# Kernel tuning notes

Hardware: AMD Instinct MI355X
Metric: run time of the kernel (lower is better)

The kernel has to match this reference:

```python
import jax, jax.numpy as jnp
import numpy as np

N = 100000      # nodes
E = 1600000     # edges
HID = 128
NODE_IN = 32
EDGE_IN = 16
EMB = 32
VOCAB = 100000
LAYERS = 3
EPS = 1e-5


def setup_inputs() -> dict:
    key = jax.random.key(0)
    ks = jax.random.split(key, 24)
    s = 0.05
    inp = {
        "x": jax.random.normal(ks[0], (N, NODE_IN), jnp.float32),
        "edge_attr": jax.random.normal(ks[1], (E, EDGE_IN), jnp.float32),
        "naics_emb": jax.random.normal(ks[2], (VOCAB, EMB), jnp.float32) * s,
        "ln_g": jnp.ones((EMB,), jnp.float32),
        "ln_b": jnp.zeros((EMB,), jnp.float32),
        "W_in": jax.random.normal(ks[3], (EMB + NODE_IN, HID), jnp.float32) * s,
        "b_in": jnp.zeros((HID,), jnp.float32),
        "Wl": jax.random.normal(ks[4], (LAYERS, HID, HID), jnp.float32) * s,
        "bl": jnp.zeros((LAYERS, HID), jnp.float32),
        "Wr": jax.random.normal(ks[5], (LAYERS, HID, HID), jnp.float32) * s,
        "bn_g": jnp.ones((LAYERS, HID), jnp.float32),
        "bn_b": jnp.zeros((LAYERS, HID), jnp.float32),
        "We1": jax.random.normal(ks[6], (2 * HID + EDGE_IN, HID), jnp.float32) * s,
        "be1": jnp.zeros((HID,), jnp.float32),
        "We2": jax.random.normal(ks[7], (HID, HID // 2), jnp.float32) * s,
        "be2": jnp.zeros((HID // 2,), jnp.float32),
        "We3": jax.random.normal(ks[8], (HID // 2, 1), jnp.float32) * s,
        "be3": jnp.zeros((1,), jnp.float32),
        "edge_index": jax.random.randint(ks[9], (2, E), 0, N, jnp.int64 if jax.config.jax_enable_x64 else jnp.int32),
        "naics_indices": jax.random.randint(ks[10], (N,), 0, VOCAB, jnp.int64 if jax.config.jax_enable_x64 else jnp.int32),
    }
    return inp


def reference(x, edge_attr, naics_emb, ln_g, ln_b, W_in, b_in, Wl, bl, Wr,
              bn_g, bn_b, We1, be1, We2, be2, We3, be3, edge_index, naics_indices):
    # NAICS embedding + LayerNorm
    emb = naics_emb[naics_indices]                    # [N, EMB]
    mu = emb.mean(-1, keepdims=True)
    var = emb.var(-1, keepdims=True)
    emb = (emb - mu) * jax.lax.rsqrt(var + EPS) * ln_g + ln_b

    # input projection (dropout in eval mode = identity)
    h = jax.nn.relu(jnp.concatenate([emb, x], axis=1) @ W_in + b_in)  # [N, HID]
    initial = h

    row, col = edge_index[0], edge_index[1]           # src, dst (PyG: aggregate at dst)
    deg = jax.ops.segment_sum(jnp.ones((E,), h.dtype), col, num_segments=N)
    inv_deg = (1.0 / jnp.maximum(deg, 1.0))[:, None]  # [N,1]

    for i in range(LAYERS):
        # SAGEConv: lin_l(mean_j x_j) + lin_r(x_i)
        agg = jax.ops.segment_sum(h[row], col, num_segments=N) * inv_deg
        out = agg @ Wl[i] + bl[i] + h @ Wr[i]
        # BatchNorm1d (training-mode batch statistics over nodes)
        m = out.mean(0)
        v = out.var(0)
        out = (out - m) * jax.lax.rsqrt(v + EPS) * bn_g[i] + bn_b[i]
        h = jnp.tanh(out) + h                         # activation + residual
        if i % 2 == 1:
            h = h + initial

    # edge-gather MLP
    ef = jnp.concatenate([h[row], h[col], edge_attr], axis=1)  # [E, 2H+EDGE_IN]
    z = jax.nn.relu(ef @ We1 + be1)
    z = jax.nn.relu(z @ We2 + be2)
    return z @ We3 + be3                              # [E, 1]
```

## Files before the change

### kernel.cpp

```cpp
#include <hip/hip_runtime.h>
#include <hip/hip_bf16.h>
#include <cstddef>

#define HID 128
#define EMBD 32
#define NIN 32
#define EIN 16
#define EPSV 1e-5f

__device__ __forceinline__ float rlf(float v, int l) {
    return __int_as_float(__builtin_amdgcn_readlane(__float_as_int(v), l));
}

extern "C" __global__ void __launch_bounds__(256)
k_input(const float* __restrict__ x, const float* __restrict__ etab,
        const int* __restrict__ nidx, const float* __restrict__ lng_,
        const float* __restrict__ lnb_, const float* __restrict__ Win,
        const float* __restrict__ bin_, float* __restrict__ h,
        float* __restrict__ init_, int* __restrict__ zi, int* __restrict__ zc, int nn)
{
    __shared__ float Ws[64 * HID];
    __shared__ float lng[EMBD], lnb[EMBD], bin[HID];
    __shared__ float xbuf[4][64];
    if (zi) {
        int gid = blockIdx.x * blockDim.x + threadIdx.x, st = gridDim.x * blockDim.x;
        for (int i = gid; i < nn; i += st) { zi[i] = 0; zc[i] = 0; }
    }
    for (int i = threadIdx.x; i < 64 * HID; i += 256) Ws[i] = Win[i];
    if (threadIdx.x < EMBD) { lng[threadIdx.x] = lng_[threadIdx.x]; lnb[threadIdx.x] = lnb_[threadIdx.x]; }
    if (threadIdx.x < HID) bin[threadIdx.x] = bin_[threadIdx.x];
    __syncthreads();
    const int wv = threadIdx.x >> 6, lane = threadIdx.x & 63;
    const int w0 = blockIdx.x * 4 + wv, nw = gridDim.x * 4;
    for (int n = w0; n < nn; n += nw) {
        float e = 0.f;
        if (lane < EMBD) e = etab[(size_t)nidx[n] * EMBD + lane];
        float s = e, q = e * e;
        #pragma unroll
        for (int o = 16; o; o >>= 1) { s += __shfl_xor(s, o, 32); q += __shfl_xor(q, o, 32); }
        if (lane < EMBD) {
            float m = s * (1.f / EMBD);
            float v = q * (1.f / EMBD) - m * m;
            xbuf[wv][lane] = (e - m) * rsqrtf(v + EPSV) * lng[lane] + lnb[lane];
        } else {
            xbuf[wv][lane] = x[(size_t)n * NIN + (lane - NIN)];
        }
        float2 a0 = *(const float2*)&bin[2 * lane], a1 = {0.f, 0.f};
        #pragma unroll 8
        for (int k = 0; k < 64; k += 2) {
            float2 wA = *(const float2*)&Ws[k * HID + 2 * lane];
            float2 wB = *(const float2*)&Ws[(k + 1) * HID + 2 * lane];
            a0.x = fmaf(xbuf[wv][k], wA.x, a0.x);     a0.y = fmaf(xbuf[wv][k], wA.y, a0.y);
            a1.x = fmaf(xbuf[wv][k + 1], wB.x, a1.x); a1.y = fmaf(xbuf[wv][k + 1], wB.y, a1.y);
        }
        float2 r; r.x = fmaxf(a0.x + a1.x, 0.f); r.y = fmaxf(a0.y + a1.y, 0.f);
        *(float2*)&h[(size_t)n * HID + 2 * lane] = r;
        *(float2*)&init_[(size_t)n * HID + 2 * lane] = r;
    }
}

extern "C" __global__ void k_deg(const int* __restrict__ col, int* __restrict__ degi, int ne) {
    int i = blockIdx.x * blockDim.x + threadIdx.x, st = gridDim.x * blockDim.x;
    for (; i < ne; i += st) atomicAdd(&degi[col[i]], 1);
}

extern "C" __global__ void __launch_bounds__(1024)
k_scan(const int* __restrict__ degi, int* __restrict__ offs, int nn) {
    __shared__ int ps[1024];
    const int t = threadIdx.x;
    const int per = (nn + 1023) / 1024;
    const int s = min(t * per, nn), e = min(s + per, nn);
    int sum = 0;
    for (int i = s; i < e; i++) sum += degi[i];
    ps[t] = sum;
    __syncthreads();
    for (int off = 1; off < 1024; off <<= 1) {
        int v = (t >= off) ? ps[t - off] : 0;
        __syncthreads();
        ps[t] += v;
        __syncthreads();
    }
    int run = (t ? ps[t - 1] : 0);
    for (int i = s; i < e; i++) { offs[i] = run; run += degi[i]; }
    if (t == 1023) offs[nn] = run;
}

extern "C" __global__ void k_fill(const int* __restrict__ row, const int* __restrict__ col,
                                  const int* __restrict__ offs, int* __restrict__ cur,
                                  int* __restrict__ csr, int ne) {
    int i = blockIdx.x * blockDim.x + threadIdx.x, st = gridDim.x * blockDim.x;
    for (; i < ne; i += st) {
        int c = col[i];
        int p = atomicAdd(&cur[c], 1);
        csr[offs[c] + p] = row[i];
    }
}

extern "C" __global__ void __launch_bounds__(256)
k_agg(const float* __restrict__ h, const int* __restrict__ offs,
      const int* __restrict__ csr, float* __restrict__ agg,
      float* __restrict__ stats, int nn)
{
    if (blockIdx.x == 0 && threadIdx.x < 2 * HID) stats[threadIdx.x] = 0.f;
    const int lane = threadIdx.x & 63;
    int w = blockIdx.x * 4 + (threadIdx.x >> 6), nw = gridDim.x * 4;
    for (int n = w; n < nn; n += nw) {
        const int o0 = offs[n], o1 = offs[n + 1];
        float2 acc0 = {0.f, 0.f}, acc1 = {0.f, 0.f};
        int j = o0;
        for (; j + 8 <= o1; j += 8) {
            int s[8];
            #pragma unroll
            for (int i = 0; i < 8; i++) s[i] = csr[j + i];
            float2 v[8];
            #pragma unroll
            for (int i = 0; i < 8; i++) v[i] = *(const float2*)&h[(size_t)s[i] * HID + 2 * lane];
            #pragma unroll
            for (int i = 0; i < 8; i += 2) {
                acc0.x += v[i].x;     acc0.y += v[i].y;
                acc1.x += v[i + 1].x; acc1.y += v[i + 1].y;
            }
        }
        for (; j < o1; j++) {
            int s0 = csr[j];
            float2 v0 = *(const float2*)&h[(size_t)s0 * HID + 2 * lane];
            acc0.x += v0.x; acc0.y += v0.y;
        }
        const float idg = 1.f / fmaxf((float)(o1 - o0), 1.f);
        float2 r; r.x = (acc0.x + acc1.x) * idg; r.y = (acc0.y + acc1.y) * idg;
        *(float2*)&agg[(size_t)n * HID + 2 * lane] = r;
    }
}

extern "C" __global__ void k_degf(const int* __restrict__ col, float* __restrict__ deg, int ne) {
    int i = blockIdx.x * blockDim.x + threadIdx.x, st = gridDim.x * blockDim.x;
    for (; i < ne; i += st) unsafeAtomicAdd(&deg[col[i]], 1.f);
}
extern "C" __global__ void k_invdeg(const float* __restrict__ deg, float* __restrict__ inv, int nn) {
    int i = blockIdx.x * blockDim.x + threadIdx.x;
    if (i < nn) inv[i] = 1.f / fmaxf(deg[i], 1.f);
}
extern "C" __global__ void __launch_bounds__(256)
k_scatter(const float* __restrict__ h, const int* __restrict__ row,
          const int* __restrict__ col, float* agg, float* __restrict__ stats, int ne)
{
    if (blockIdx.x == 0 && threadIdx.x < 2 * HID) stats[threadIdx.x] = 0.f;
    const int lane = threadIdx.x & 63;
    int w = blockIdx.x * 4 + (threadIdx.x >> 6), nw = gridDim.x * 4;
    for (int e = w; e < ne; e += nw) {
        int r = row[e], c = col[e];
        float2 v = *(const float2*)&h[(size_t)r * HID + 2 * lane];
        unsafeAtomicAdd(&agg[(size_t)c * HID + 2 * lane], v.x);
        unsafeAtomicAdd(&agg[(size_t)c * HID + 2 * lane + 1], v.y);
    }
}

extern "C" __global__ void __launch_bounds__(512)
k_gemm(const float* __restrict__ X1, const float* __restrict__ scale,
       const float* __restrict__ W1, const float* __restrict__ X2,
       const float* __restrict__ W2, const float* __restrict__ bias,
       float* __restrict__ out, float* __restrict__ stats, int nn)
{
    __shared__ float W1s[HID * HID];
    __shared__ float W2s[HID * HID];
    const int tid = threadIdx.x;
    const bool dual = (X2 != nullptr);
    for (int i = tid; i < HID * HID / 4; i += 512) {
        ((float4*)W1s)[i] = ((const float4*)W1)[i];
        if (dual) ((float4*)W2s)[i] = ((const float4*)W2)[i];
    }
    __syncthreads();
    const int lane = tid & 63, wv = tid >> 6;
    const int gw = blockIdx.x * 8 + wv, nwv = gridDim.x * 8;
    float2 bv = {0.f, 0.f};
    if (bias) bv = *(const float2*)&bias[2 * lane];
    float2 sm = {0.f, 0.f}, sq = {0.f, 0.f};
    for (int nb = gw * 8; nb < nn; nb += nwv * 8) {
        const int nN = min(8, nn - nb);
        float2 xA[8], xB[8];
        #pragma unroll
        for (int i = 0; i < 8; i++) {
            xA[i] = {0.f, 0.f}; xB[i] = {0.f, 0.f};
            if (i < nN) {
                xA[i] = *(const float2*)&X1[(size_t)(nb + i) * HID + 2 * lane];
                if (scale) { float sc = scale[nb + i]; xA[i].x *= sc; xA[i].y *= sc; }
                if (dual) xB[i] = *(const float2*)&X2[(size_t)(nb + i) * HID + 2 * lane];
            }
        }
        float2 acc[8];
        #pragma unroll
        for (int i = 0; i < 8; i++) acc[i] = bv;
        if (dual) {
            for (int k = 0; k < HID; k += 2) {
                float2 w1a = *(const float2*)&W1s[k * HID + 2 * lane];
                float2 w1b = *(const float2*)&W1s[(k + 1) * HID + 2 * lane];
                float2 w2a = *(const float2*)&W2s[k * HID + 2 * lane];
                float2 w2b = *(const float2*)&W2s[(k + 1) * HID + 2 * lane];
                const int kl = k >> 1;
                #pragma unroll
                for (int i = 0; i < 8; i++) {
                    float sa = rlf(xA[i].x, kl), sb = rlf(xA[i].y, kl);
                    float ta = rlf(xB[i].x, kl), tb = rlf(xB[i].y, kl);
                    acc[i].x = fmaf(sa, w1a.x, acc[i].x); acc[i].y = fmaf(sa, w1a.y, acc[i].y);
                    acc[i].x = fmaf(sb, w1b.x, acc[i].x); acc[i].y = fmaf(sb, w1b.y, acc[i].y);
                    acc[i].x = fmaf(ta, w2a.x, acc[i].x); acc[i].y = fmaf(ta, w2a.y, acc[i].y);
                    acc[i].x = fmaf(tb, w2b.x, acc[i].x); acc[i].y = fmaf(tb, w2b.y, acc[i].y);
                }
            }
        } else {
            for (int k = 0; k < HID; k += 2) {
                float2 w1a = *(const float2*)&W1s[k * HID + 2 * lane];
                float2 w1b = *(const float2*)&W1s[(k + 1) * HID + 2 * lane];
                const int kl = k >> 1;
                #pragma unroll
                for (int i = 0; i < 8; i++) {
                    float sa = rlf(xA[i].x, kl), sb = rlf(xA[i].y, kl);
                    acc[i].x = fmaf(sa, w1a.x, acc[i].x); acc[i].y = fmaf(sa, w1a.y, acc[i].y);
                    acc[i].x = fmaf(sb, w1b.x, acc[i].x); acc[i].y = fmaf(sb, w1b.y, acc[i].y);
                }
            }
        }
        #pragma unroll
        for (int i = 0; i < 8; i++) {
            if (i < nN) {
                *(float2*)&out[(size_t)(nb + i) * HID + 2 * lane] = acc[i];
                sm.x += acc[i].x; sm.y += acc[i].y;
                sq.x += acc[i].x * acc[i].x; sq.y += acc[i].y * acc[i].y;
            }
        }
    }
    unsafeAtomicAdd(&stats[2 * lane],           sm.x);
    unsafeAtomicAdd(&stats[2 * lane + 1],       sm.y);
    unsafeAtomicAdd(&stats[HID + 2 * lane],     sq.x);
    unsafeAtomicAdd(&stats[HID + 2 * lane + 1], sq.y);
}

extern "C" __global__ void __launch_bounds__(256)
k_update(const float* __restrict__ outb, const float* __restrict__ stats,
         const float* __restrict__ g, const float* __restrict__ b,
         float* h, const float* __restrict__ init_, int addinit, int n4, float invn)
{
    __shared__ float scsh[2 * HID];
    if (threadIdx.x < HID) {
        int f = threadIdx.x;
        float m = stats[f] * invn;
        float v = stats[HID + f] * invn - m * m;
        float s = rsqrtf(v + EPSV) * g[f];
        scsh[f] = s;
        scsh[HID + f] = fmaf(-m, s, b[f]);
    }
    __syncthreads();
    int i = blockIdx.x * blockDim.x + threadIdx.x, st = gridDim.x * blockDim.x;
    for (; i < n4; i += st) {
        float4 o = ((const float4*)outb)[i];
        int f = (i & 31) * 4;
        float4 s  = *(const float4*)&scsh[f];
        float4 sh = *(const float4*)&scsh[HID + f];
        float4 hv = ((const float4*)h)[i];
        float4 r;
        r.x = tanhf(fmaf(o.x, s.x, sh.x)) + hv.x;
        r.y = tanhf(fmaf(o.y, s.y, sh.y)) + hv.y;
        r.z = tanhf(fmaf(o.z, s.z, sh.z)) + hv.z;
        r.w = tanhf(fmaf(o.w, s.w, sh.w)) + hv.w;
        if (addinit) {
            float4 iv = ((const float4*)init_)[i];
            r.x += iv.x; r.y += iv.y; r.z += iv.z; r.w += iv.w;
        }
        ((float4*)h)[i] = r;
    }
}

extern "C" __global__ void __launch_bounds__(512)
k_proj(const float* __restrict__ outb, const float* __restrict__ stats,
       const float* __restrict__ g, const float* __restrict__ b,
       const float* __restrict__ hold, const float* __restrict__ W1,
       const float* __restrict__ W2, const float* __restrict__ b1,
       float* __restrict__ outA, float* __restrict__ outB, int nn, float invn)
{
    __shared__ float W1s[HID * HID];
    __shared__ float W2s[HID * HID];
    __shared__ float scsh[2 * HID];
    const int tid = threadIdx.x;
    for (int i = tid; i < HID * HID / 4; i += 512) {
        ((float4*)W1s)[i] = ((const float4*)W1)[i];
        ((float4*)W2s)[i] = ((const float4*)W2)[i];
    }
    if (tid < HID) {
        float m = stats[tid] * invn;
        float v = stats[HID + tid] * invn - m * m;
        float s = rsqrtf(v + EPSV) * g[tid];
        scsh[tid] = s;
        scsh[HID + tid] = fmaf(-m, s, b[tid]);
    }
    __syncthreads();
    const int lane = tid & 63, wv = tid >> 6;
    const int gw = blockIdx.x * 8 + wv, nwv = gridDim.x * 8;
    const float2 sA  = *(const float2*)&scsh[2 * lane];
    const float2 shA = *(const float2*)&scsh[HID + 2 * lane];
    float2 bv = *(const float2*)&b1[2 * lane];
    for (int nb = gw * 8; nb < nn; nb += nwv * 8) {
        const int nN = min(8, nn - nb);
        float2 xH[8];
        #pragma unroll
        for (int i = 0; i < 8; i++) {
            xH[i] = {0.f, 0.f};
            if (i < nN) {
                float2 o  = *(const float2*)&outb[(size_t)(nb + i) * HID + 2 * lane];
                float2 hv = *(const float2*)&hold[(size_t)(nb + i) * HID + 2 * lane];
                xH[i].x = tanhf(fmaf(o.x, sA.x, shA.x)) + hv.x;
                xH[i].y = tanhf(fmaf(o.y, sA.y, shA.y)) + hv.y;
            }
        }
        float2 accA[8], accB[8];
        #pragma unroll
        for (int i = 0; i < 8; i++) { accA[i] = bv; accB[i] = {0.f, 0.f}; }
        for (int k = 0; k < HID; k += 2) {
            float2 w1a = *(const float2*)&W1s[k * HID + 2 * lane];
            float2 w1b = *(const float2*)&W1s[(k + 1) * HID + 2 * lane];
            float2 w2a = *(const float2*)&W2s[k * HID + 2 * lane];
            float2 w2b = *(const float2*)&W2s[(k + 1) * HID + 2 * lane];
            const int kl = k >> 1;
            #pragma unroll
            for (int i = 0; i < 8; i++) {
                float sa = rlf(xH[i].x, kl), sb = rlf(xH[i].y, kl);
                accA[i].x = fmaf(sa, w1a.x, accA[i].x); accA[i].y = fmaf(sa, w1a.y, accA[i].y);
                accA[i].x = fmaf(sb, w1b.x, accA[i].x); accA[i].y = fmaf(sb, w1b.y, accA[i].y);
                accB[i].x = fmaf(sa, w2a.x, accB[i].x); accB[i].y = fmaf(sa, w2a.y, accB[i].y);
                accB[i].x = fmaf(sb, w2b.x, accB[i].x); accB[i].y = fmaf(sb, w2b.y, accB[i].y);
            }
        }
        #pragma unroll
        for (int i = 0; i < 8; i++) {
            if (i < nN) {
                *(float2*)&outA[(size_t)(nb + i) * HID + 2 * lane] = accA[i];
                *(float2*)&outB[(size_t)(nb + i) * HID + 2 * lane] = accB[i];
            }
        }
    }
}

extern "C" __global__ void __launch_bounds__(256)
k_edge(const float* __restrict__ A, const float* __restrict__ B,
       const float* __restrict__ eattr, const int* __restrict__ row,
       const int* __restrict__ col, const float* __restrict__ We1e,
       const float* __restrict__ We2, const float* __restrict__ be2,
       const float* __restrict__ We3, const float* __restrict__ be3,
       float* __restrict__ outp, int beg, int end, int ne)
{
    __shared__ float zbuf[32][132];
    __shared__ float tbuf[4][32][8];
    const int tid = threadIdx.x, lane = tid & 63, wv = tid >> 6;
    float2 w1r[16];
    #pragma unroll
    for (int j = 0; j < 16; j++) w1r[j] = *(const float2*)&We1e[j * HID + 2 * lane];
    const int fi = lane & 7, ks = lane >> 3;
    const int f0 = 16 * wv + 2 * fi;
    float w2r0[16], w2r1[16];
    #pragma unroll
    for (int m = 0; m < 16; m++) {
        w2r0[m] = We2[(16 * ks + m) * 64 + f0];
        w2r1[m] = We2[(16 * ks + m) * 64 + f0 + 1];
    }
    const float b20 = be2[f0], b21 = be2[f0 + 1];
    const float w30 = We3[f0], w31 = We3[f0 + 1];
    const float bias3 = be3[0];
    const int wcol4 = (((lane >> 1) & 3) << 3) | ((lane >> 1) >> 2);
    const int woff = wcol4 * 4 + (lane & 1) * 2;
    for (int cb = beg + blockIdx.x * 32; cb < end; cb += gridDim.x * 32) {
        const int e0 = cb + wv * 8;
        float2 ear = {0.f, 0.f};
        if (e0 + (lane >> 3) < ne) ear = *(const float2*)&eattr[(size_t)e0 * EIN + 2 * lane];
        int rr[8], cc[8];
        #pragma unroll
        for (int i = 0; i < 8; i++) {
            const int e = e0 + i;
            rr[i] = (e < ne) ? row[e] : 0;
            cc[i] = (e < ne) ? col[e] : 0;
        }
        float2 av[8], bv8[8];
        #pragma unroll
        for (int i = 0; i < 8; i++) {
            av[i]  = *(const float2*)&A[(size_t)rr[i] * HID + 2 * lane];
            bv8[i] = *(const float2*)&B[(size_t)cc[i] * HID + 2 * lane];
        }
        float* zw = &zbuf[wv * 8][woff];
        #pragma unroll
        for (int i = 0; i < 8; i++) {
            float2 q; q.x = av[i].x + bv8[i].x; q.y = av[i].y + bv8[i].y;
            #pragma unroll
            for (int j = 0; j < 16; j++) {
                float s = rlf((j & 1) ? ear.y : ear.x, i * 8 + (j >> 1));
                q.x = fmaf(s, w1r[j].x, q.x);
                q.y = fmaf(s, w1r[j].y, q.y);
            }
            q.x = fmaxf(q.x, 0.f); q.y = fmaxf(q.y, 0.f);
            *(float2*)zw = q;
            zw += 132;
        }
        __syncthreads();
        const float* zp = &zbuf[0][ks * 4];
        #pragma unroll 2
        for (int e = 0; e < 32; e++) {
            float4 z0 = *(const float4*)(zp);
            float4 z1 = *(const float4*)(zp + 32);
            float4 z2 = *(const float4*)(zp + 64);
            float4 z3 = *(const float4*)(zp + 96);
            zp += 132;
            float acc0 = 0.f, acc1 = 0.f;
            acc0 = fmaf(z0.x, w2r0[0],  acc0); acc1 = fmaf(z0.x, w2r1[0],  acc1);
            acc0 = fmaf(z0.y, w2r0[1],  acc0); acc1 = fmaf(z0.y, w2r1[1],  acc1);
            acc0 = fmaf(z0.z, w2r0[2],  acc0); acc1 = fmaf(z0.z, w2r1[2],  acc1);
            acc0 = fmaf(z0.w, w2r0[3],  acc0); acc1 = fmaf(z0.w, w2r1[3],  acc1);
            acc0 = fmaf(z1.x, w2r0[4],  acc0); acc1 = fmaf(z1.x, w2r1[4],  acc1);
            acc0 = fmaf(z1.y, w2r0[5],  acc0); acc1 = fmaf(z1.y, w2r1[5],  acc1);
            acc0 = fmaf(z1.z, w2r0[6],  acc0); acc1 = fmaf(z1.z, w2r1[6],  acc1);
            acc0 = fmaf(z1.w, w2r0[7],  acc0); acc1 = fmaf(z1.w, w2r1[7],  acc1);
            acc0 = fmaf(z2.x, w2r0[8],  acc0); acc1 = fmaf(z2.x, w2r1[8],  acc1);
            acc0 = fmaf(z2.y, w2r0[9],  acc0); acc1 = fmaf(z2.y, w2r1[9],  acc1);
            acc0 = fmaf(z2.z, w2r0[10], acc0); acc1 = fmaf(z2.z, w2r1[10], acc1);
            acc0 = fmaf(z2.w, w2r0[11], acc0); acc1 = fmaf(z2.w, w2r1[11], acc1);
            acc0 = fmaf(z3.x, w2r0[12], acc0); acc1 = fmaf(z3.x, w2r1[12], acc1);
            acc0 = fmaf(z3.y, w2r0[13], acc0); acc1 = fmaf(z3.y, w2r1[13], acc1);
            acc0 = fmaf(z3.z, w2r0[14], acc0); acc1 = fmaf(z3.z, w2r1[14], acc1);
            acc0 = fmaf(z3.w, w2r0[15], acc0); acc1 = fmaf(z3.w, w2r1[15], acc1);
            acc0 += __shfl_xor(acc0, 8);  acc1 += __shfl_xor(acc1, 8);
            acc0 += __shfl_xor(acc0, 16); acc1 += __shfl_xor(acc1, 16);
            acc0 += __shfl_xor(acc0, 32); acc1 += __shfl_xor(acc1, 32);
            float o0 = fmaxf(acc0 + b20, 0.f), o1 = fmaxf(acc1 + b21, 0.f);
            float t3 = fmaf(o0, w30, o1 * w31);
            if (ks == 0) tbuf[wv][e][fi] = t3;
        }
        __syncthreads();
        {
            const int e = tid >> 3, p = tid & 7;
            float s = (tbuf[0][e][p] + tbuf[1][e][p]) + (tbuf[2][e][p] + tbuf[3][e][p]);
            s += __shfl_xor(s, 1); s += __shfl_xor(s, 2); s += __shfl_xor(s, 4);
            if (p == 0 && cb + e < end) outp[cb + e] = s + bias3;
        }
        __syncthreads();
    }
}

extern "C" void kernel_launch(void* const* d_in, const int* in_sizes, int n_in,
                              void* d_out, int out_size, void* d_ws, size_t ws_size,
                              hipStream_t stream)
{
    const float* x     = (const float*)d_in[0];
    const float* eattr = (const float*)d_in[1];
    const float* etab  = (const float*)d_in[2];
    const float* lng   = (const float*)d_in[3];
    const float* lnb   = (const float*)d_in[4];
    const float* Win   = (const float*)d_in[5];
    const float* bin   = (const float*)d_in[6];
    const float* Wl    = (const float*)d_in[7];
    const float* bl    = (const float*)d_in[8];
    const float* Wr    = (const float*)d_in[9];
    const float* bng   = (const float*)d_in[10];
    const float* bnb   = (const float*)d_in[11];
    const float* We1   = (const float*)d_in[12];
    const float* be1   = (const float*)d_in[13];
    const float* We2   = (const float*)d_in[14];
    const float* be2   = (const float*)d_in[15];
    const float* We3   = (const float*)d_in[16];
    const float* be3   = (const float*)d_in[17];
    const int*   eidx  = (const int*)d_in[18];
    const int*   nidx  = (const int*)d_in[19];

    const int nn = in_sizes[0] / NIN;
    const int ne = in_sizes[1] / EIN;
    const int* row = eidx;
    const int* col = eidx + ne;
    const float invn = 1.0f / nn;

    float* ws = (float*)d_ws;
    const size_t big = (size_t)nn * HID;
    float* h    = ws;
    float* bufB = ws + big;
    float* bufA = ws + 2 * big;
    float* tail = ws + 3 * big;

    const size_t need_csr = (3 * big + 3 * (size_t)nn + 1 + (size_t)ne + 512) * 4;
    const bool use_csr = (ws_size >= need_csr);

    if (use_csr) {
        int*   degi  = (int*)tail;
        int*   offs  = degi + nn;
        int*   cur   = offs + nn + 1;
        int*   csr   = cur + nn;
        float* stats = (float*)(csr + ne);

        k_input<<<512, 256, 0, stream>>>(x, etab, nidx, lng, lnb, Win, bin, h, bufB,
                                         degi, cur, nn);
        k_deg<<<1024, 256, 0, stream>>>(col, degi, ne);
        k_scan<<<1, 1024, 0, stream>>>(degi, offs, nn);
        k_fill<<<1024, 256, 0, stream>>>(row, col, offs, cur, csr, ne);

        for (int i = 0; i < 3; i++) {
            k_agg<<<2048, 256, 0, stream>>>(h, offs, csr, bufA, stats, nn);
            k_gemm<<<256, 512, 0, stream>>>(bufA, nullptr, Wl + (size_t)i * HID * HID,
                                            h, Wr + (size_t)i * HID * HID, bl + i * HID,
                                            bufA, stats, nn);
            if (i < 2) {
                k_update<<<1024, 256, 0, stream>>>(bufA, stats, bng + i * HID, bnb + i * HID,
                                                   h, bufB, i & 1, nn * HID / 4, invn);
            } else {
                k_proj<<<256, 512, 0, stream>>>(bufA, stats, bng + i * HID, bnb + i * HID,
                                                h, We1, We1 + HID * HID, be1,
                                                bufA, bufB, nn, invn);
            }
        }
    } else {
        float* deg   = tail;
        float* inv   = deg + nn;
        float* stats = inv + nn;

        k_input<<<512, 256, 0, stream>>>(x, etab, nidx, lng, lnb, Win, bin, h, bufB,
                                         nullptr, nullptr, nn);
        hipMemsetAsync(deg, 0, (size_t)nn * 4, stream);
        k_degf<<<1024, 256, 0, stream>>>(col, deg, ne);
        k_invdeg<<<(nn + 255) / 256, 256, 0, stream>>>(deg, inv, nn);

        for (int i = 0; i < 3; i++) {
            hipMemsetAsync(bufA, 0, big * 4, stream);
            k_scatter<<<2048, 256, 0, stream>>>(h, row, col, bufA, stats, ne);
            k_gemm<<<256, 512, 0, stream>>>(bufA, inv, Wl + (size_t)i * HID * HID,
                                            h, Wr + (size_t)i * HID * HID, bl + i * HID,
                                            bufA, stats, nn);
            if (i < 2) {
                k_update<<<1024, 256, 0, stream>>>(bufA, stats, bng + i * HID, bnb + i * HID,
                                                   h, bufB, i & 1, nn * HID / 4, invn);
            } else {
                k_proj<<<256, 512, 0, stream>>>(bufA, stats, bng + i * HID, bnb + i * HID,
                                                h, We1, We1 + HID * HID, be1,
                                                bufA, bufB, nn, invn);
            }
        }
    }

    const int half = (ne / 2) & ~31;
    k_edge<<<1792, 256, 0, stream>>>(bufA, bufB, eattr, row, col,
                                     We1 + 2 * HID * HID, We2, be2, We3, be3,
                                     (float*)d_out, 0, half, ne);
    k_edge<<<1792, 256, 0, stream>>>(bufA, bufB, eattr, row, col,
                                     We1 + 2 * HID * HID, We2, be2, We3, be3,
                                     (float*)d_out, half, ne, ne);
}
```

Measured before the change: 2.897 ms.

## Widen node GEMM blocks to 768 threads and re-split edge MLP second layer

The node GEMM and projection kernels go from 512 to 768 threads per block, so each block that stages the two 128x128 weight matrices in shared memory runs twelve waves instead of eight. This amortises the weight load over more rows and adds waves per CU. In the edge kernel, the second-layer work is re-split: each wave now covers 32 output features over 16 edges, each lane reduces over 32 inputs instead of 16, and one shuffle stage is dropped. The cost is more registers per lane (64 held weights) and tighter register limits at 768 threads, which could cause spills or lower occupancy.

Result: faster. 2.685 ms (-7.3%).

```diff
diff --git a/kernel.cpp b/kernel.cpp
--- a/kernel.cpp
+++ b/kernel.cpp
@@ -155,7 +155,7 @@
     }
 }
 
-extern "C" __global__ void __launch_bounds__(512)
+extern "C" __global__ void __launch_bounds__(768)
 k_gemm(const float* __restrict__ X1, const float* __restrict__ scale,
        const float* __restrict__ W1, const float* __restrict__ X2,
        const float* __restrict__ W2, const float* __restrict__ bias,
@@ -165,13 +165,13 @@
     __shared__ float W2s[HID * HID];
     const int tid = threadIdx.x;
     const bool dual = (X2 != nullptr);
-    for (int i = tid; i < HID * HID / 4; i += 512) {
+    for (int i = tid; i < HID * HID / 4; i += 768) {
         ((float4*)W1s)[i] = ((const float4*)W1)[i];
         if (dual) ((float4*)W2s)[i] = ((const float4*)W2)[i];
     }
     __syncthreads();
     const int lane = tid & 63, wv = tid >> 6;
-    const int gw = blockIdx.x * 8 + wv, nwv = gridDim.x * 8;
+    const int gw = blockIdx.x * 12 + wv, nwv = gridDim.x * 12;
     float2 bv = {0.f, 0.f};
     if (bias) bv = *(const float2*)&bias[2 * lane];
     float2 sm = {0.f, 0.f}, sq = {0.f, 0.f};
@@ -270,7 +270,7 @@
     }
 }
 
-extern "C" __global__ void __launch_bounds__(512)
+extern "C" __global__ void __launch_bounds__(768)
 k_proj(const float* __restrict__ outb, const float* __restrict__ stats,
        const float* __restrict__ g, const float* __restrict__ b,
        const float* __restrict__ hold, const float* __restrict__ W1,
@@ -281,7 +281,7 @@
     __shared__ float W2s[HID * HID];
     __shared__ float scsh[2 * HID];
     const int tid = threadIdx.x;
-    for (int i = tid; i < HID * HID / 4; i += 512) {
+    for (int i = tid; i < HID * HID / 4; i += 768) {
         ((float4*)W1s)[i] = ((const float4*)W1)[i];
         ((float4*)W2s)[i] = ((const float4*)W2)[i];
     }
@@ -294,7 +294,7 @@
     }
     __syncthreads();
     const int lane = tid & 63, wv = tid >> 6;
-    const int gw = blockIdx.x * 8 + wv, nwv = gridDim.x * 8;
+    const int gw = blockIdx.x * 12 + wv, nwv = gridDim.x * 12;
     const float2 sA  = *(const float2*)&scsh[2 * lane];
     const float2 shA = *(const float2*)&scsh[HID + 2 * lane];
     float2 bv = *(const float2*)&b1[2 * lane];
@@ -348,18 +348,20 @@
        float* __restrict__ outp, int beg, int end, int ne)
 {
     __shared__ float zbuf[32][132];
-    __shared__ float tbuf[4][32][8];
+    __shared__ float tbuf[2][32][16];
     const int tid = threadIdx.x, lane = tid & 63, wv = tid >> 6;
     float2 w1r[16];
     #pragma unroll
     for (int j = 0; j < 16; j++) w1r[j] = *(const float2*)&We1e[j * HID + 2 * lane];
-    const int fi = lane & 7, ks = lane >> 3;
-    const int f0 = 16 * wv + 2 * fi;
-    float w2r0[16], w2r1[16];
+    const int fi = lane & 15, ks = lane >> 4;
+    const int fh = wv & 1;
+    const int ebase = (wv >> 1) * 16;
+    const int f0 = 32 * fh + 2 * fi;
+    float w2r0[32], w2r1[32];
     #pragma unroll
-    for (int m = 0; m < 16; m++) {
-        w2r0[m] = We2[(16 * ks + m) * 64 + f0];
-        w2r1[m] = We2[(16 * ks + m) * 64 + f0 + 1];
+    for (int m = 0; m < 32; m++) {
+        w2r0[m] = We2[(32 * ks + m) * 64 + f0];
+        w2r1[m] = We2[(32 * ks + m) * 64 + f0 + 1];
     }
     const float b20 = be2[f0], b21 = be2[f0 + 1];
     const float w30 = We3[f0], w31 = We3[f0 + 1];
@@ -398,42 +400,39 @@
             zw += 132;
         }
         __syncthreads();
-        const float* zp = &zbuf[0][ks * 4];
+        const float* zq = &zbuf[ebase][8 * ks];
+#define FQ(Z, M) \
+            acc0 = fmaf(Z.x, w2r0[M],     acc0); acc1 = fmaf(Z.x, w2r1[M],     acc1); \
+            acc0 = fmaf(Z.y, w2r0[(M)+1], acc0); acc1 = fmaf(Z.y, w2r1[(M)+1], acc1); \
+            acc0 = fmaf(Z.z, w2r0[(M)+2], acc0); acc1 = fmaf(Z.z, w2r1[(M)+2], acc1); \
+            acc0 = fmaf(Z.w, w2r0[(M)+3], acc0); acc1 = fmaf(Z.w, w2r1[(M)+3], acc1);
         #pragma unroll 2
-        for (int e = 0; e < 32; e++) {
-            float4 z0 = *(const float4*)(zp);
-            float4 z1 = *(const float4*)(zp + 32);
-            float4 z2 = *(const float4*)(zp + 64);
-            float4 z3 = *(const float4*)(zp + 96);
-            zp += 132;
+        for (int e2 = 0; e2 < 16; e2++) {
+            float4 z0 = *(const float4*)(zq);
+            float4 z1 = *(const float4*)(zq + 32);
+            float4 z2 = *(const float4*)(zq + 64);
+            float4 z3 = *(const float4*)(zq + 96);
+            float4 z4 = *(const float4*)(zq + 4);
+            float4 z5 = *(const float4*)(zq + 36);
+            float4 z6 = *(const float4*)(zq + 68);
+            float4 z7 = *(const float4*)(zq + 100);
+            zq += 132;
             float acc0 = 0.f, acc1 = 0.f;
-            acc0 = fmaf(z0.x, w2r0[0],  acc0); acc1 = fmaf(z0.x, w2r1[0],  acc1);
-            acc0 = fmaf(z0.y, w2r0[1],  acc0); acc1 = fmaf(z0.y, w2r1[1],  acc1);
-            acc0 = fmaf(z0.z, w2r0[2],  acc0); acc1 = fmaf(z0.z, w2r1[2],  acc1);
-            acc0 = fmaf(z0.w, w2r0[3],  acc0); acc1 = fmaf(z0.w, w2r1[3],  acc1);
-            acc0 = fmaf(z1.x, w2r0[4],  acc0); acc1 = fmaf(z1.x, w2r1[4],  acc1);
-            acc0 = fmaf(z1.y, w2r0[5],  acc0); acc1 = fmaf(z1.y, w2r1[5],  acc1);
-            acc0 = fmaf(z1.z, w2r0[6],  acc0); acc1 = fmaf(z1.z, w2r1[6],  acc1);
-            acc0 = fmaf(z1.w, w2r0[7],  acc0); acc1 = fmaf(z1.w, w2r1[7],  acc1);
-            acc0 = fmaf(z2.x, w2r0[8],  acc0); acc1 = fmaf(z2.x, w2r1[8],  acc1);
-            acc0 = fmaf(z2.y, w2r0[9],  acc0); acc1 = fmaf(z2.y, w2r1[9],  acc1);
-            acc0 = fmaf(z2.z, w2r0[10], acc0); acc1 = fmaf(z2.z, w2r1[10], acc1);
-            acc0 = fmaf(z2.w, w2r0[11], acc0); acc1 = fmaf(z2.w, w2r1[11], acc1);
-            acc0 = fmaf(z3.x, w2r0[12], acc0); acc1 = fmaf(z3.x, w2r1[12], acc1);
-            acc0 = fmaf(z3.y, w2r0[13], acc0); acc1 = fmaf(z3.y, w2r1[13], acc1);
-            acc0 = fmaf(z3.z, w2r0[14], acc0); acc1 = fmaf(z3.z, w2r1[14], acc1);
-            acc0 = fmaf(z3.w, w2r0[15], acc0); acc1 = fmaf(z3.w, w2r1[15], acc1);
-            acc0 += __shfl_xor(acc0, 8);  acc1 += __shfl_xor(acc1, 8);
+            FQ(z0, 0)  FQ(z1, 4)  FQ(z2, 8)  FQ(z3, 12)
+            FQ(z4, 16) FQ(z5, 20) FQ(z6, 24) FQ(z7, 28)
             acc0 += __shfl_xor(acc0, 16); acc1 += __shfl_xor(acc1, 16);
             acc0 += __shfl_xor(acc0, 32); acc1 += __shfl_xor(acc1, 32);
-            float o0 = fmaxf(acc0 + b20, 0.f), o1 = fmaxf(acc1 + b21, 0.f);
-            float t3 = fmaf(o0, w30, o1 * w31);
-            if (ks == 0) tbuf[wv][e][fi] = t3;
-        }
+            if (ks == 0) {
+                float o0 = fmaxf(acc0 + b20, 0.f), o1 = fmaxf(acc1 + b21, 0.f);
+                tbuf[fh][ebase + e2][fi] = fmaf(o0, w30, o1 * w31);
+            }
+        }
+#undef FQ
         __syncthreads();
         {
             const int e = tid >> 3, p = tid & 7;
-            float s = (tbuf[0][e][p] + tbuf[1][e][p]) + (tbuf[2][e][p] + tbuf[3][e][p]);
+            float s = (tbuf[0][e][p] + tbuf[0][e][p + 8]) +
+                      (tbuf[1][e][p] + tbuf[1][e][p + 8]);
             s += __shfl_xor(s, 1); s += __shfl_xor(s, 2); s += __shfl_xor(s, 4);
             if (p == 0 && cb + e < end) outp[cb + e] = s + bias3;
         }
@@ -497,14 +496,14 @@
 
         for (int i = 0; i < 3; i++) {
             k_agg<<<2048, 256, 0, stream>>>(h, offs, csr, bufA, stats, nn);
-            k_gemm<<<256, 512, 0, stream>>>(bufA, nullptr, Wl + (size_t)i * HID * HID,
+            k_gemm<<<256, 768, 0, stream>>>(bufA, nullptr, Wl + (size_t)i * HID * HID,
                                             h, Wr + (size_t)i * HID * HID, bl + i * HID,
                                             bufA, stats, nn);
             if (i < 2) {
                 k_update<<<1024, 256, 0, stream>>>(bufA, stats, bng + i * HID, bnb + i * HID,
                                                    h, bufB, i & 1, nn * HID / 4, invn);
             } else {
-                k_proj<<<256, 512, 0, stream>>>(bufA, stats, bng + i * HID, bnb + i * HID,
+                k_proj<<<256, 768, 0, stream>>>(bufA, stats, bng + i * HID, bnb + i * HID,
                                                 h, We1, We1 + HID * HID, be1,
                                                 bufA, bufB, nn, invn);
             }
@@ -523,14 +522,14 @@
         for (int i = 0; i < 3; i++) {
             hipMemsetAsync(bufA, 0, big * 4, stream);
             k_scatter<<<2048, 256, 0, stream>>>(h, row, col, bufA, stats, ne);
-            k_gemm<<<256, 512, 0, stream>>>(bufA, inv, Wl + (size_t)i * HID * HID,
+            k_gemm<<<256, 768, 0, stream>>>(bufA, inv, Wl + (size_t)i * HID * HID,
                                             h, Wr + (size_t)i * HID * HID, bl + i * HID,
                                             bufA, stats, nn);
             if (i < 2) {
                 k_update<<<1024, 256, 0, stream>>>(bufA, stats, bng + i * HID, bnb + i * HID,
                                                    h, bufB, i & 1, nn * HID / 4, invn);
             } else {
-                k_proj<<<256, 512, 0, stream>>>(bufA, stats, bng + i * HID, bnb + i * HID,
+                k_proj<<<256, 768, 0, stream>>>(bufA, stats, bng + i * HID, bnb + i * HID,
                                                 h, We1, We1 + HID * HID, be1,
                                                 bufA, bufB, nn, invn);
             }
```
